# Kernel optimization log

Measured on AMD Instinct MI355X. Metric: run time of the kernel, lower is better.

## Reference

```python
import jax, jax.numpy as jnp
import numpy as np

M, K, L, C = 8, 4, 2, 128
C_v = C // M


def _bilinear(img, gx, gy):
    # img: [N, C_v, h, w]; gx, gy: [N, K, H, W] normalized grid coords in [-1, 1]
    # torch F.grid_sample(mode='bilinear', padding_mode='zeros', align_corners=False)
    N, Cc, h, w = img.shape
    ix = ((gx + 1.0) * w - 1.0) * 0.5
    iy = ((gy + 1.0) * h - 1.0) * 0.5
    x0 = jnp.floor(ix)
    y0 = jnp.floor(iy)
    wx1 = ix - x0
    wy1 = iy - y0
    wx0 = 1.0 - wx1
    wy0 = 1.0 - wy1

    def gather(xs, ys):
        valid = ((xs >= 0) & (xs < w) & (ys >= 0) & (ys < h)).astype(img.dtype)
        xc = jnp.clip(xs, 0, w - 1).astype(jnp.int32)
        yc = jnp.clip(ys, 0, h - 1).astype(jnp.int32)
        v = jax.vmap(lambda im, y, x: im[:, y, x])(img, yc, xc)  # [N, C_v, K, H, W]
        return v * valid[:, None]

    out = (gather(x0, y0) * (wx0 * wy0)[:, None]
           + gather(x0 + 1.0, y0) * (wx1 * wy0)[:, None]
           + gather(x0, y0 + 1.0) * (wx0 * wy1)[:, None]
           + gather(x0 + 1.0, y0 + 1.0) * (wx1 * wy1)[:, None])
    return out  # [N, C_v, K, H, W]


def _forward(z_q, x0, x1, p_q, Wq, bq, Wd, bd, Wa, ba, Wp, bp, Wm, bm):
    B, H, W, _ = z_q.shape
    zq = z_q @ Wq + bq
    # sampling offsets and attention weights
    deltas = (zq @ Wd + bd).reshape(B, H, W, M, L, K, 2)
    A = jax.nn.softmax((zq @ Wa + ba).reshape(B, H, W, M, L * K), axis=-1)
    # deltas -> [B*M, L, K, H, W, 2]; A -> [B*M, H*W, L*K]
    d = jnp.transpose(deltas, (0, 3, 4, 5, 1, 2, 6)).reshape(B * M, L, K, H, W, 2)
    An = jnp.transpose(A, (0, 3, 1, 2, 4)).reshape(B * M, H * W, L * K)
    pq = jax.lax.stop_gradient(p_q)  # phi() detaches p_q in the original

    samples = []
    for l, xl in enumerate([x0, x1]):
        h, w = xl.shape[1], xl.shape[2]
        phi = pq * jnp.array([w - 1.0, h - 1.0], dtype=z_q.dtype)  # phi(w,h,p_q)
        # NOTE: torch .repeat(M,1,1,1) tiles batch as m*B+b (replicated faithfully)
        phi = jnp.tile(phi, (M, 1, 1, 1))  # [M*B, H, W, 2]
        Wx = (xl @ Wp + bp).reshape(B, h, w, M, C_v)
        Wx = jnp.transpose(Wx, (0, 3, 4, 1, 2)).reshape(B * M, C_v, h, w)
        coords = phi[:, None] + d[:, l]  # [B*M, K, H, W, 2]
        gx = 2.0 * coords[..., 0] / max(w - 1, 1) - 1.0
        gy = 2.0 * coords[..., 1] / max(h - 1, 1) - 1.0
        s = _bilinear(Wx, gx, gy)  # [B*M, C_v, K, H, W]
        # original stacks per-k samples at dim=3 -> [B*M, C_v, H, K, W]
        samples.append(jnp.transpose(s, (0, 1, 3, 2, 4)))
    S = jnp.stack(samples, axis=1)  # [B*M, L, C_v, H, K, W]
    # faithful to original permute(0,4,5,3,1,2).view(B*M, H*W, C_v, L*K)
    S = jnp.transpose(S, (0, 4, 5, 3, 1, 2)).reshape(B * M, H * W, C_v, L * K)
    out = jnp.einsum('nlds,nls->nld', S, An)  # [B*M, H*W, C_v]
    out = out.reshape(B, M, H, W, C_v)
    out = jnp.transpose(out, (0, 2, 3, 1, 4)).reshape(B, H, W, M * C_v)
    return out @ Wm + bm


def setup_inputs() -> dict:
    key = jax.random.key(0)
    ks = jax.random.split(key, 14)
    B, H, W = 2, 128, 128
    s = 0.02
    return {
        'z_q': jax.random.normal(ks[0], (B, H, W, C), jnp.float32),
        'x0': jax.random.normal(ks[1], (B, 64, 64, C), jnp.float32),
        'x1': jax.random.normal(ks[2], (B, 128, 128, C), jnp.float32),
        'p_q': jax.random.uniform(ks[3], (B, H, W, 2), jnp.float32),
        'Wq': jax.random.normal(ks[4], (C, C), jnp.float32) * s,
        'bq': jnp.zeros((C,), jnp.float32),
        'Wd': jax.random.normal(ks[5], (C, 2 * M * K * L), jnp.float32) * s,
        'bd': jax.random.normal(ks[6], (2 * M * K * L,), jnp.float32),
        'Wa': jax.random.normal(ks[7], (C, M * K * L), jnp.float32) * s,
        'ba': jnp.full((M * K * L,), 1.0 / (L * K), jnp.float32),
        'Wp': jax.random.normal(ks[8], (C, C), jnp.float32) * s,
        'bp': jnp.zeros((C,), jnp.float32),
        'Wm': jax.random.normal(ks[9], (C, C), jnp.float32) * s,
        'bm': jnp.zeros((C,), jnp.float32),
    }


def reference(z_q, x0, x1, p_q, Wq, bq, Wd, bd, Wa, ba, Wp, bp, Wm, bm):
    return _forward(z_q, x0, x1, p_q, Wq, bq, Wd, bd, Wa, ba, Wp, bp, Wm, bm)
```

## Files before the change

### kernel.cpp

```cpp
#include <hip/hip_runtime.h>
#include <hip/hip_bf16.h>

constexpr int CB = 2;
constexpr int CH = 128;
constexpr int CW = 128;
constexpr int CM = 8;

typedef __bf16 bf16x8 __attribute__((ext_vector_type(8)));
typedef float  f32x4  __attribute__((ext_vector_type(4)));
typedef unsigned short us8 __attribute__((ext_vector_type(8)));

__device__ __forceinline__ unsigned short f2bf(float f) {
  __hip_bfloat16 h = __float2bfloat16(f);
  return *reinterpret_cast<unsigned short*>(&h);
}
__device__ __forceinline__ float bf2f(unsigned short u) {
  __hip_bfloat16 h;
  *reinterpret_cast<unsigned short*>(&h) = u;
  return __bfloat162float(h);
}

__global__ __launch_bounds__(256) void prep_all_kernel(
    const float* __restrict__ Wq, const float* __restrict__ bq,
    const float* __restrict__ Wd, const float* __restrict__ bd,
    const float* __restrict__ Wa, const float* __restrict__ ba,
    const float* __restrict__ Wp, const float* __restrict__ Wm,
    unsigned short* __restrict__ WtDA, unsigned short* __restrict__ WtP,
    unsigned short* __restrict__ WtM, float* __restrict__ bda)
{
  const int blk = blockIdx.x, t = threadIdx.x;
  if (blk < 96) {
    const int idx = blk * 256 + t;
    const int j = idx >> 7, k = idx & 127;
    float s = 0.f;
    if (j < 128) {
      for (int i = 0; i < 128; ++i) s = fmaf(Wq[k * 128 + i], Wd[i * 128 + j], s);
    } else {
      for (int i = 0; i < 128; ++i) s = fmaf(Wq[k * 128 + i], Wa[i * 64 + (j - 128)], s);
    }
    WtDA[j * 128 + k] = f2bf(s);
  } else if (blk < 224) {
    const int idx = (blk - 96) * 256 + t;
    if (idx < 16384) {
      const int k = idx >> 7, j = idx & 127;
      WtP[j * 128 + k] = f2bf(Wp[idx]);
    } else {
      const int i2 = idx - 16384;
      const int k = i2 >> 7, j = i2 & 127;
      WtM[j * 128 + k] = f2bf(Wm[i2]);
    }
  } else {
    if (t < 192) {
      const int j = t;
      float s = (j < 128) ? bd[j] : ba[j - 128];
      if (j < 128) {
        for (int i = 0; i < 128; ++i) s = fmaf(bq[i], Wd[i * 128 + j], s);
      } else {
        for (int i = 0; i < 128; ++i) s = fmaf(bq[i], Wa[i * 64 + (j - 128)], s);
      }
      bda[j] = s;
    }
  }
}

__global__ __launch_bounds__(256) void pre_gemm_kernel(
    const float* __restrict__ z_q, const float* __restrict__ x0,
    const float* __restrict__ x1,
    const unsigned short* __restrict__ WtDA, const float* __restrict__ bda,
    const unsigned short* __restrict__ WtP,  const float* __restrict__ bp,
    float* __restrict__ dl2, float* __restrict__ Alog,
    unsigned short* __restrict__ Wx, int nZ)
{
  const int t  = threadIdx.x;
  const int w  = t >> 6;
  const int l  = t & 63;
  const int lr = l & 15;
  const int kg = l >> 4;
  const int blk = blockIdx.x;

  if (blk < nZ) {
    const int r0 = blk * 64;
    const float* Ap = z_q + (size_t)(r0 + w * 16 + lr) * 128 + kg * 8;

    f32x4 acc[12];
#pragma unroll
    for (int jt = 0; jt < 12; ++jt) acc[jt] = (f32x4){0.f, 0.f, 0.f, 0.f};

#pragma unroll
    for (int k0 = 0; k0 < 128; k0 += 32) {
      const float4 f0 = *(const float4*)(Ap + k0);
      const float4 f1 = *(const float4*)(Ap + k0 + 4);
      const float ff[8] = {f0.x, f0.y, f0.z, f0.w, f1.x, f1.y, f1.z, f1.w};
      us8 uh;
#pragma unroll
      for (int i = 0; i < 8; ++i) uh[i] = f2bf(ff[i]);
      const bf16x8 ah = __builtin_bit_cast(bf16x8, uh);

      const unsigned short* Wk = WtDA + lr * 128 + k0 + kg * 8;
#pragma unroll
      for (int jt = 0; jt < 12; ++jt) {
        const bf16x8 bh = *(const bf16x8*)(Wk + jt * 16 * 128);
        acc[jt] = __builtin_amdgcn_mfma_f32_16x16x32_bf16(ah, bh, acc[jt], 0, 0, 0);
      }
    }

    const int scol = ((lr >> 1) & 3) * 32 + ((lr >> 3) & 1) * 2 + (lr & 1);
#pragma unroll
    for (int jt = 0; jt < 8; ++jt) {
      const float bv = bda[jt * 16 + lr];
#pragma unroll
      for (int rg = 0; rg < 4; ++rg) {
        const int row = r0 + w * 16 + kg * 4 + rg;
        dl2[(size_t)row * 128 + jt * 4 + scol] = acc[jt][rg] + bv;
      }
    }
#pragma unroll
    for (int jt = 8; jt < 12; ++jt) {
      const int col = (jt - 8) * 16 + lr;
      const float bv = bda[128 + col];
#pragma unroll
      for (int rg = 0; rg < 4; ++rg) {
        const int row = r0 + w * 16 + kg * 4 + rg;
        Alog[(size_t)row * 64 + col] = acc[jt][rg] + bv;
      }
    }
  } else {
    const int r0 = (blk - nZ) * 64;
    const float* A = (r0 < 8192) ? (x0 + (size_t)r0 * 128)
                                 : (x1 + (size_t)(r0 - 8192) * 128);
    const float* Ap = A + (size_t)(w * 16 + lr) * 128 + kg * 8;

    f32x4 acc[8];
#pragma unroll
    for (int jt = 0; jt < 8; ++jt) acc[jt] = (f32x4){0.f, 0.f, 0.f, 0.f};

#pragma unroll
    for (int k0 = 0; k0 < 128; k0 += 32) {
      const float4 f0 = *(const float4*)(Ap + k0);
      const float4 f1 = *(const float4*)(Ap + k0 + 4);
      const float ff[8] = {f0.x, f0.y, f0.z, f0.w, f1.x, f1.y, f1.z, f1.w};
      us8 uh, ul;
#pragma unroll
      for (int i = 0; i < 8; ++i) {
        const unsigned short hi = f2bf(ff[i]);
        uh[i] = hi;
        ul[i] = f2bf(ff[i] - bf2f(hi));
      }
      const bf16x8 ah = __builtin_bit_cast(bf16x8, uh);
      const bf16x8 al = __builtin_bit_cast(bf16x8, ul);

      const unsigned short* Wk = WtP + lr * 128 + k0 + kg * 8;
#pragma unroll
      for (int jt = 0; jt < 8; ++jt) {
        const bf16x8 bh = *(const bf16x8*)(Wk + jt * 16 * 128);
        acc[jt] = __builtin_amdgcn_mfma_f32_16x16x32_bf16(ah, bh, acc[jt], 0, 0, 0);
        acc[jt] = __builtin_amdgcn_mfma_f32_16x16x32_bf16(al, bh, acc[jt], 0, 0, 0);
      }
    }

#pragma unroll
    for (int jt = 0; jt < 8; ++jt) {
      const int col = jt * 16 + lr;
      const float bv = bp[col];
#pragma unroll
      for (int rg = 0; rg < 4; ++rg) {
        const int row = r0 + w * 16 + kg * 4 + rg;
        Wx[(size_t)row * 128 + col] = f2bf(acc[jt][rg] + bv);
      }
    }
  }
}

__global__ __launch_bounds__(256) void final_gemm_kernel(
    const unsigned short* __restrict__ Pbf,
    const unsigned short* __restrict__ WtM,
    const float* __restrict__ bm, float* __restrict__ out)
{
  const int t  = threadIdx.x;
  const int w  = t >> 6;
  const int l  = t & 63;
  const int lr = l & 15;
  const int kg = l >> 4;
  const int r0 = blockIdx.x * 64;

  const unsigned short* Ap = Pbf + (size_t)(r0 + w * 16 + lr) * 128 + kg * 8;

  f32x4 acc[8];
#pragma unroll
  for (int jt = 0; jt < 8; ++jt) acc[jt] = (f32x4){0.f, 0.f, 0.f, 0.f};

#pragma unroll
  for (int k0 = 0; k0 < 128; k0 += 32) {
    const bf16x8 av = *(const bf16x8*)(Ap + k0);
    const unsigned short* Wk = WtM + lr * 128 + k0 + kg * 8;
#pragma unroll
    for (int jt = 0; jt < 8; ++jt) {
      const bf16x8 bh = *(const bf16x8*)(Wk + jt * 16 * 128);
      acc[jt] = __builtin_amdgcn_mfma_f32_16x16x32_bf16(av, bh, acc[jt], 0, 0, 0);
    }
  }

#pragma unroll
  for (int jt = 0; jt < 8; ++jt) {
    const int col = jt * 16 + lr;
    const float bv = bm[col];
#pragma unroll
    for (int rg = 0; rg < 4; ++rg) {
      const int row = r0 + w * 16 + kg * 4 + rg;
      out[(size_t)row * 128 + col] = acc[jt][rg] + bv;
    }
  }
}

__global__ __launch_bounds__(128) void sample_attn_kernel(
    const float* __restrict__ Alog,
    const float* __restrict__ dl2,
    const float* __restrict__ p_q,
    const unsigned short* __restrict__ Wx,
    unsigned short* __restrict__ Pbf)
{
  const int q = blockIdx.x;
  const int w = q & (CW - 1);
  const int h = (q >> 7) & (CH - 1);
  const int b = q >> 14;
  const int t = threadIdx.x;
  const int m = t >> 4;
  const int c = t & 15;

  const int kk   = h >> 5;
  const int xp   = (w >> 5) + ((h & 31) << 2);
  const int yp   = (c >> 2) + ((w & 31) << 2);
  const int lp   = (c >> 1) & 1;
  const int half = c & 1;

  const size_t qp = ((size_t)b * CH + yp) * CW + xp;
  const float2 dxy = *(const float2*)(dl2 + qp * 128 + kk * 32 + m * 4 + lp * 2);

  const int pb = (b * CM + m) % CB;
  const float2 pq2 = *(const float2*)(p_q + ((((size_t)pb * CH + yp) * CW + xp) * 2));

  const float* al = Alog + (size_t)q * 64 + m * 8;
  const float4 al0 = ((const float4*)al)[0];
  const float4 al1 = ((const float4*)al)[1];

  const int wl = lp ? 128 : 64;
  const int hl = wl;
  const int imgbase = lp ? (8192 + b * 16384) : (b * 4096);

  const float cx = pq2.x * (float)(wl - 1) + dxy.x;
  const float cy = pq2.y * (float)(hl - 1) + dxy.y;
  const float gx = 2.f * cx / (float)(wl - 1) - 1.f;
  const float gy = 2.f * cy / (float)(hl - 1) - 1.f;
  const float ix = ((gx + 1.f) * (float)wl - 1.f) * 0.5f;
  const float iy = ((gy + 1.f) * (float)hl - 1.f) * 0.5f;
  const float x0f = floorf(ix), y0f = floorf(iy);
  const float fx1 = ix - x0f, fy1 = iy - y0f;
  const float fx0 = 1.f - fx1, fy0 = 1.f - fy1;
  const int xi = (int)x0f, yi = (int)y0f;

  const float vx0 = ((unsigned)xi < (unsigned)wl) ? 1.f : 0.f;
  const float vx1 = ((unsigned)(xi + 1) < (unsigned)wl) ? 1.f : 0.f;
  const float vy0 = ((unsigned)yi < (unsigned)hl) ? 1.f : 0.f;
  const float vy1 = ((unsigned)(yi + 1) < (unsigned)hl) ? 1.f : 0.f;
  const int xc0 = min(max(xi, 0), wl - 1);
  const int xc1 = min(max(xi + 1, 0), wl - 1);
  const int yc0 = min(max(yi, 0), hl - 1);
  const int yc1 = min(max(yi + 1, 0), hl - 1);

  const unsigned short* base = Wx + (size_t)imgbase * 128 + (m * 16 + half * 8);
  const unsigned short* p00 = base + (size_t)(yc0 * wl + xc0) * 128;
  const unsigned short* p01 = base + (size_t)(yc0 * wl + xc1) * 128;
  const unsigned short* p10 = base + (size_t)(yc1 * wl + xc0) * 128;
  const unsigned short* p11 = base + (size_t)(yc1 * wl + xc1) * 128;

  const us8 g00 = *(const us8*)p00;
  const us8 g01 = *(const us8*)p01;
  const us8 g10 = *(const us8*)p10;
  const us8 g11 = *(const us8*)p11;

  float lg[8] = {al0.x, al0.y, al0.z, al0.w, al1.x, al1.y, al1.z, al1.w};
  float mx = -3.0e38f;
#pragma unroll
  for (int s = 0; s < 8; ++s) mx = fmaxf(mx, lg[s]);
  float se = 0.f;
#pragma unroll
  for (int s = 0; s < 8; ++s) { lg[s] = __expf(lg[s] - mx); se += lg[s]; }
  const float inv = 1.f / se;

  const float w00 = fy0 * fx0 * vy0 * vx0;
  const float w01 = fy0 * fx1 * vy0 * vx1;
  const float w10 = fy1 * fx0 * vy1 * vx0;
  const float w11 = fy1 * fx1 * vy1 * vx1;

  float acc[8];
#pragma unroll
  for (int s = 0; s < 8; ++s) {
    float v = w00 * bf2f(g00[s]);
    v = fmaf(w01, bf2f(g01[s]), v);
    v = fmaf(w10, bf2f(g10[s]), v);
    v = fmaf(w11, bf2f(g11[s]), v);
    acc[s] = v;
  }

  float o = 0.f;
#pragma unroll
  for (int s = 0; s < 8; ++s) o = fmaf(lg[s] * inv, acc[s], o);
  Pbf[(size_t)q * 128 + t] = f2bf(o);
}

extern "C" void kernel_launch(void* const* d_in, const int* in_sizes, int n_in,
                              void* d_out, int out_size, void* d_ws, size_t ws_size,
                              hipStream_t stream)
{
  const float* z_q = (const float*)d_in[0];
  const float* x0  = (const float*)d_in[1];
  const float* x1  = (const float*)d_in[2];
  const float* p_q = (const float*)d_in[3];
  const float* Wq  = (const float*)d_in[4];
  const float* bq  = (const float*)d_in[5];
  const float* Wd  = (const float*)d_in[6];
  const float* bd  = (const float*)d_in[7];
  const float* Wa  = (const float*)d_in[8];
  const float* ba  = (const float*)d_in[9];
  const float* Wp  = (const float*)d_in[10];
  const float* bp  = (const float*)d_in[11];
  const float* Wm  = (const float*)d_in[12];
  const float* bm  = (const float*)d_in[13];

  float* ws = (float*)d_ws;
  const int NQ = CB * CH * CW;

  unsigned short* Wts  = (unsigned short*)ws;
  unsigned short* WtDA = Wts;
  unsigned short* WtP  = Wts + 24576;
  unsigned short* WtM  = Wts + 40960;
  float* bda = ws + 28672;

  float* dl2  = ws + 28864;
  float* Alog = dl2 + 4194304;
  unsigned short* Wx  = (unsigned short*)(Alog + 2097152);
  unsigned short* Pbf = Wx + 5242880;

  prep_all_kernel<<<225, 256, 0, stream>>>(Wq, bq, Wd, bd, Wa, ba, Wp, Wm,
                                           WtDA, WtP, WtM, bda);

  const int nZ = NQ / 64;
  pre_gemm_kernel<<<nZ + 640, 256, 0, stream>>>(z_q, x0, x1, WtDA, bda,
                                                WtP, bp, dl2, Alog, Wx, nZ);

  sample_attn_kernel<<<NQ, 128, 0, stream>>>(Alog, dl2, p_q, Wx, Pbf);

  final_gemm_kernel<<<NQ / 64, 256, 0, stream>>>(Pbf, WtM, bm, (float*)d_out);
}
```

Before: 200.0 us.

## Fuse output projection into sampling kernel and retile pre-GEMM to 32 rows

Removes the separate final GEMM kernel and the bf16 Pbf intermediate. Each sampling block now stages its 128-channel result in shared memory and does the Wm projection with scalar FMAs per thread, reading bf16 weights directly. The pre-GEMM tiles shrink from 64 to 32 rows per block, with waves split across column groups, which doubles the grid and lowers register pressure. It also adds a bit-shift bf16-to-float conversion and unrolls the prep loops. The cost is that the output projection moves from MFMA to scalar math, with 128 FMAs per thread and repeated WtM reads per query.

```diff
diff --git a/kernel.cpp b/kernel.cpp
--- a/kernel.cpp
+++ b/kernel.cpp
@@ -15,9 +15,9 @@
   return *reinterpret_cast<unsigned short*>(&h);
 }
 __device__ __forceinline__ float bf2f(unsigned short u) {
-  __hip_bfloat16 h;
-  *reinterpret_cast<unsigned short*>(&h) = u;
-  return __bfloat162float(h);
+  union { unsigned int i; float f; } v;
+  v.i = ((unsigned int)u) << 16;
+  return v.f;
 }
 
 __global__ __launch_bounds__(256) void prep_all_kernel(
@@ -34,8 +34,10 @@
     const int j = idx >> 7, k = idx & 127;
     float s = 0.f;
     if (j < 128) {
+#pragma unroll 8
       for (int i = 0; i < 128; ++i) s = fmaf(Wq[k * 128 + i], Wd[i * 128 + j], s);
     } else {
+#pragma unroll 8
       for (int i = 0; i < 128; ++i) s = fmaf(Wq[k * 128 + i], Wa[i * 64 + (j - 128)], s);
     }
     WtDA[j * 128 + k] = f2bf(s);
@@ -54,8 +56,10 @@
       const int j = t;
       float s = (j < 128) ? bd[j] : ba[j - 128];
       if (j < 128) {
+#pragma unroll 8
         for (int i = 0; i < 128; ++i) s = fmaf(bq[i], Wd[i * 128 + j], s);
       } else {
+#pragma unroll 8
         for (int i = 0; i < 128; ++i) s = fmaf(bq[i], Wa[i * 64 + (j - 128)], s);
       }
       bda[j] = s;
@@ -71,20 +75,23 @@
     float* __restrict__ dl2, float* __restrict__ Alog,
     unsigned short* __restrict__ Wx, int nZ)
 {
-  const int t  = threadIdx.x;
-  const int w  = t >> 6;
-  const int l  = t & 63;
-  const int lr = l & 15;
-  const int kg = l >> 4;
+  const int t   = threadIdx.x;
+  const int wv  = t >> 6;
+  const int l   = t & 63;
+  const int lr  = l & 15;
+  const int kg  = l >> 4;
+  const int rgp = wv >> 1;
+  const int cg  = wv & 1;
   const int blk = blockIdx.x;
 
   if (blk < nZ) {
-    const int r0 = blk * 64;
-    const float* Ap = z_q + (size_t)(r0 + w * 16 + lr) * 128 + kg * 8;
-
-    f32x4 acc[12];
-#pragma unroll
-    for (int jt = 0; jt < 12; ++jt) acc[jt] = (f32x4){0.f, 0.f, 0.f, 0.f};
+    const int r0 = blk * 32;
+    const int arow = r0 + rgp * 16 + lr;
+    const float* Ap = z_q + (size_t)arow * 128 + kg * 8;
+
+    f32x4 acc[6];
+#pragma unroll
+    for (int jt = 0; jt < 6; ++jt) acc[jt] = (f32x4){0.f, 0.f, 0.f, 0.f};
 
 #pragma unroll
     for (int k0 = 0; k0 < 128; k0 += 32) {
@@ -96,43 +103,44 @@
       for (int i = 0; i < 8; ++i) uh[i] = f2bf(ff[i]);
       const bf16x8 ah = __builtin_bit_cast(bf16x8, uh);
 
-      const unsigned short* Wk = WtDA + lr * 128 + k0 + kg * 8;
-#pragma unroll
-      for (int jt = 0; jt < 12; ++jt) {
-        const bf16x8 bh = *(const bf16x8*)(Wk + jt * 16 * 128);
+#pragma unroll
+      for (int jt = 0; jt < 6; ++jt) {
+        const int col = (cg * 6 + jt) * 16 + lr;
+        const bf16x8 bh = *(const bf16x8*)(WtDA + col * 128 + k0 + kg * 8);
         acc[jt] = __builtin_amdgcn_mfma_f32_16x16x32_bf16(ah, bh, acc[jt], 0, 0, 0);
       }
     }
 
     const int scol = ((lr >> 1) & 3) * 32 + ((lr >> 3) & 1) * 2 + (lr & 1);
 #pragma unroll
-    for (int jt = 0; jt < 8; ++jt) {
-      const float bv = bda[jt * 16 + lr];
-#pragma unroll
-      for (int rg = 0; rg < 4; ++rg) {
-        const int row = r0 + w * 16 + kg * 4 + rg;
-        dl2[(size_t)row * 128 + jt * 4 + scol] = acc[jt][rg] + bv;
-      }
-    }
-#pragma unroll
-    for (int jt = 8; jt < 12; ++jt) {
-      const int col = (jt - 8) * 16 + lr;
-      const float bv = bda[128 + col];
-#pragma unroll
-      for (int rg = 0; rg < 4; ++rg) {
-        const int row = r0 + w * 16 + kg * 4 + rg;
-        Alog[(size_t)row * 64 + col] = acc[jt][rg] + bv;
+    for (int jt = 0; jt < 6; ++jt) {
+      const int jtg = cg * 6 + jt;
+      if (jtg < 8) {
+        const float bv = bda[jtg * 16 + lr];
+#pragma unroll
+        for (int ri = 0; ri < 4; ++ri) {
+          const int row = r0 + rgp * 16 + kg * 4 + ri;
+          dl2[(size_t)row * 128 + jtg * 4 + scol] = acc[jt][ri] + bv;
+        }
+      } else {
+        const int col = (jtg - 8) * 16 + lr;
+        const float bv = bda[128 + col];
+#pragma unroll
+        for (int ri = 0; ri < 4; ++ri) {
+          const int row = r0 + rgp * 16 + kg * 4 + ri;
+          Alog[(size_t)row * 64 + col] = acc[jt][ri] + bv;
+        }
       }
     }
   } else {
-    const int r0 = (blk - nZ) * 64;
+    const int r0 = (blk - nZ) * 32;
     const float* A = (r0 < 8192) ? (x0 + (size_t)r0 * 128)
                                  : (x1 + (size_t)(r0 - 8192) * 128);
-    const float* Ap = A + (size_t)(w * 16 + lr) * 128 + kg * 8;
-
-    f32x4 acc[8];
-#pragma unroll
-    for (int jt = 0; jt < 8; ++jt) acc[jt] = (f32x4){0.f, 0.f, 0.f, 0.f};
+    const float* Ap = A + (size_t)(rgp * 16 + lr) * 128 + kg * 8;
+
+    f32x4 acc[4];
+#pragma unroll
+    for (int jt = 0; jt < 4; ++jt) acc[jt] = (f32x4){0.f, 0.f, 0.f, 0.f};
 
 #pragma unroll
     for (int k0 = 0; k0 < 128; k0 += 32) {
@@ -149,76 +157,39 @@
       const bf16x8 ah = __builtin_bit_cast(bf16x8, uh);
       const bf16x8 al = __builtin_bit_cast(bf16x8, ul);
 
-      const unsigned short* Wk = WtP + lr * 128 + k0 + kg * 8;
-#pragma unroll
-      for (int jt = 0; jt < 8; ++jt) {
-        const bf16x8 bh = *(const bf16x8*)(Wk + jt * 16 * 128);
+#pragma unroll
+      for (int jt = 0; jt < 4; ++jt) {
+        const int col = (cg * 4 + jt) * 16 + lr;
+        const bf16x8 bh = *(const bf16x8*)(WtP + col * 128 + k0 + kg * 8);
         acc[jt] = __builtin_amdgcn_mfma_f32_16x16x32_bf16(ah, bh, acc[jt], 0, 0, 0);
         acc[jt] = __builtin_amdgcn_mfma_f32_16x16x32_bf16(al, bh, acc[jt], 0, 0, 0);
       }
     }
 
 #pragma unroll
-    for (int jt = 0; jt < 8; ++jt) {
-      const int col = jt * 16 + lr;
+    for (int jt = 0; jt < 4; ++jt) {
+      const int col = (cg * 4 + jt) * 16 + lr;
       const float bv = bp[col];
 #pragma unroll
-      for (int rg = 0; rg < 4; ++rg) {
-        const int row = r0 + w * 16 + kg * 4 + rg;
-        Wx[(size_t)row * 128 + col] = f2bf(acc[jt][rg] + bv);
+      for (int ri = 0; ri < 4; ++ri) {
+        const int row = r0 + rgp * 16 + kg * 4 + ri;
+        Wx[(size_t)row * 128 + col] = f2bf(acc[jt][ri] + bv);
       }
     }
   }
 }
 
-__global__ __launch_bounds__(256) void final_gemm_kernel(
-    const unsigned short* __restrict__ Pbf,
-    const unsigned short* __restrict__ WtM,
-    const float* __restrict__ bm, float* __restrict__ out)
-{
-  const int t  = threadIdx.x;
-  const int w  = t >> 6;
-  const int l  = t & 63;
-  const int lr = l & 15;
-  const int kg = l >> 4;
-  const int r0 = blockIdx.x * 64;
-
-  const unsigned short* Ap = Pbf + (size_t)(r0 + w * 16 + lr) * 128 + kg * 8;
-
-  f32x4 acc[8];
-#pragma unroll
-  for (int jt = 0; jt < 8; ++jt) acc[jt] = (f32x4){0.f, 0.f, 0.f, 0.f};
-
-#pragma unroll
-  for (int k0 = 0; k0 < 128; k0 += 32) {
-    const bf16x8 av = *(const bf16x8*)(Ap + k0);
-    const unsigned short* Wk = WtM + lr * 128 + k0 + kg * 8;
-#pragma unroll
-    for (int jt = 0; jt < 8; ++jt) {
-      const bf16x8 bh = *(const bf16x8*)(Wk + jt * 16 * 128);
-      acc[jt] = __builtin_amdgcn_mfma_f32_16x16x32_bf16(av, bh, acc[jt], 0, 0, 0);
-    }
-  }
-
-#pragma unroll
-  for (int jt = 0; jt < 8; ++jt) {
-    const int col = jt * 16 + lr;
-    const float bv = bm[col];
-#pragma unroll
-    for (int rg = 0; rg < 4; ++rg) {
-      const int row = r0 + w * 16 + kg * 4 + rg;
-      out[(size_t)row * 128 + col] = acc[jt][rg] + bv;
-    }
-  }
-}
-
-__global__ __launch_bounds__(128) void sample_attn_kernel(
+__global__ __launch_bounds__(128) void sample_attn_out_kernel(
     const float* __restrict__ Alog,
     const float* __restrict__ dl2,
     const float* __restrict__ p_q,
     const unsigned short* __restrict__ Wx,
-    unsigned short* __restrict__ Pbf)
+    const unsigned short* __restrict__ WtM,
+    const float* __restrict__ bm,
+    float* __restrict__ out)
 {
+  __shared__ float Psh[128];
+
   const int q = blockIdx.x;
   const int w = q & (CW - 1);
   const int h = (q >> 7) & (CH - 1);
@@ -292,20 +263,35 @@
   const float w10 = fy1 * fx0 * vy1 * vx0;
   const float w11 = fy1 * fx1 * vy1 * vx1;
 
-  float acc[8];
+  float o = 0.f;
 #pragma unroll
   for (int s = 0; s < 8; ++s) {
     float v = w00 * bf2f(g00[s]);
     v = fmaf(w01, bf2f(g01[s]), v);
     v = fmaf(w10, bf2f(g10[s]), v);
     v = fmaf(w11, bf2f(g11[s]), v);
-    acc[s] = v;
+    o = fmaf(lg[s] * inv, v, o);
   }
-
-  float o = 0.f;
-#pragma unroll
-  for (int s = 0; s < 8; ++s) o = fmaf(lg[s] * inv, acc[s], o);
-  Pbf[(size_t)q * 128 + t] = f2bf(o);
+  Psh[t] = o;
+  __syncthreads();
+
+  float acc = bm[t];
+  const unsigned short* wc = WtM + t * 128;
+#pragma unroll
+  for (int k0 = 0; k0 < 128; k0 += 8) {
+    const us8 w8 = *(const us8*)(wc + k0);
+    const float4 pA = *(const float4*)&Psh[k0];
+    const float4 pB = *(const float4*)&Psh[k0 + 4];
+    acc = fmaf(pA.x, bf2f(w8[0]), acc);
+    acc = fmaf(pA.y, bf2f(w8[1]), acc);
+    acc = fmaf(pA.z, bf2f(w8[2]), acc);
+    acc = fmaf(pA.w, bf2f(w8[3]), acc);
+    acc = fmaf(pB.x, bf2f(w8[4]), acc);
+    acc = fmaf(pB.y, bf2f(w8[5]), acc);
+    acc = fmaf(pB.z, bf2f(w8[6]), acc);
+    acc = fmaf(pB.w, bf2f(w8[7]), acc);
+  }
+  out[(size_t)q * 128 + t] = acc;
 }
 
 extern "C" void kernel_launch(void* const* d_in, const int* in_sizes, int n_in,
@@ -339,16 +325,14 @@
   float* dl2  = ws + 28864;
   float* Alog = dl2 + 4194304;
   unsigned short* Wx  = (unsigned short*)(Alog + 2097152);
-  unsigned short* Pbf = Wx + 5242880;
 
   prep_all_kernel<<<225, 256, 0, stream>>>(Wq, bq, Wd, bd, Wa, ba, Wp, Wm,
                                            WtDA, WtP, WtM, bda);
 
-  const int nZ = NQ / 64;
-  pre_gemm_kernel<<<nZ + 640, 256, 0, stream>>>(z_q, x0, x1, WtDA, bda,
-                                                WtP, bp, dl2, Alog, Wx, nZ);
-
-  sample_attn_kernel<<<NQ, 128, 0, stream>>>(Alog, dl2, p_q, Wx, Pbf);
-
-  final_gemm_kernel<<<NQ / 64, 256, 0, stream>>>(Pbf, WtM, bm, (float*)d_out);
-}
+  const int nZ = NQ / 32;
+  pre_gemm_kernel<<<nZ + 1280, 256, 0, stream>>>(z_q, x0, x1, WtDA, bda,
+                                                 WtP, bp, dl2, Alog, Wx, nZ);
+
+  sample_attn_out_kernel<<<NQ, 128, 0, stream>>>(Alog, dl2, p_q, Wx,
+                                                 WtM, bm, (float*)d_out);
+}
```

Result: slower. 324.3 us (+62.2%).
